# Performance work log

Measured on AMD Instinct MI355X. Metric: run time of the kernel, lower is better.

Reference implementation:

```python
import jax, jax.numpy as jnp
import numpy as np

N = 50000      # number of predictions
E = 1_600_000  # total neighborhood entries (sum of neighborhood sizes)
D = 128        # prediction representation dim
A = 4          # additional per-pair info dim (box offsets / IoU)
H = 128        # block hidden dim


def setup_inputs() -> dict:
    key = jax.random.key(0)
    ks = jax.random.split(key, 16)
    interpolated = jax.random.normal(ks[0], (N, D), dtype=jnp.float32)
    add_info = jax.random.normal(ks[1], (E, A), dtype=jnp.float32)
    neighbor_idx = jax.random.randint(ks[2], (E,), 0, N, dtype=jnp.int32)
    segment_ids = jnp.sort(jax.random.randint(ks[3], (E,), 0, N, dtype=jnp.int32))
    w = lambda k, shape: (jax.random.normal(k, shape, dtype=jnp.float32) * 0.02)
    return {
        "interpolated": interpolated,
        "add_info": add_info,
        "neighbor_idx": neighbor_idx,
        "segment_ids": segment_ids,
        "Wb0": w(ks[4], (D + A, H)), "bb0": jnp.zeros((H,), jnp.float32),
        "Wo0": w(ks[5], (H, D)),     "bo0": jnp.zeros((D,), jnp.float32),
        "Wb1": w(ks[6], (D + A, H)), "bb1": jnp.zeros((H,), jnp.float32),
        "Wo1": w(ks[7], (H, D)),     "bo1": jnp.zeros((D,), jnp.float32),
        "Wf": w(ks[8], (D, 1)),      "bf": jnp.zeros((1,), jnp.float32),
    }


def reference(interpolated, add_info, neighbor_idx, segment_ids,
              Wb0, bb0, Wo0, bo0, Wb1, bb1, Wo1, bo1, Wf, bf):
    def block_step(feats, Wb, bb, Wo, bo):
        # assemble all neighborhoods: gather neighbor reps, concat pair info -> (E, D+A)
        edge_feats = jnp.concatenate([feats[neighbor_idx], add_info], axis=-1)
        # block MLP on neighborhood entries -> (E, H)
        h = jax.nn.relu(edge_feats @ Wb + bb)
        # segment-wise max pool over each prediction's neighborhood -> (N, H)
        pooled = jax.ops.segment_max(h, segment_ids, num_segments=N)
        pooled = jnp.where(jnp.isfinite(pooled), pooled, 0.0)  # empty segments -> 0
        # output projection back to representation space, residual update
        return feats + (pooled @ Wo + bo)

    x = block_step(interpolated, Wb0, bb0, Wo0, bo0)
    x = block_step(x, Wb1, bb1, Wo1, bo1)
    # final layers: compress representation to updated objectness score -> (N, 1)
    return x @ Wf + bf
```

## Files before the change

kernel.cpp:

```cpp
#include <hip/hip_runtime.h>
#include <limits.h>
#include <cstdint>

typedef __bf16 bf16_t;
typedef __attribute__((ext_vector_type(8))) __bf16 bf16x8;
typedef __attribute__((ext_vector_type(4))) float f32x4;
typedef __attribute__((ext_vector_type(2))) float f32x2;

#define CH 64

__device__ __forceinline__ float rlf(float v, int l) {
  return __int_as_float(__builtin_amdgcn_readlane(__float_as_int(v), l));
}

struct PackArgs {
  const float* W[4];
  bf16_t* P[4];
};

__global__ __launch_bounds__(256) void pack4_kernel(PackArgs args) {
  int idx = blockIdx.x * blockDim.x + threadIdx.x;
  int which = idx >> 14;
  int r = idx & 16383;
  int j  = r & 7;
  int L  = (r >> 3) & 63;
  int nt = (r >> 9) & 7;
  int kt = r >> 12;
  int k = kt * 32 + (L >> 4) * 8 + j;
  int n = nt * 16 + (L & 15);
  args.P[which][r] = (bf16_t)args.W[which][(size_t)k * 128 + n];
}

__global__ __launch_bounds__(256, 4) void yproj_f32(
    const float* __restrict__ X, const bf16_t* __restrict__ Wtpk,
    bf16_t* __restrict__ Ybf, float* __restrict__ pooled, int N)
{
  const int tid = threadIdx.x;
  const int base = blockIdx.x * 128;

  float4 z = make_float4(0.f, 0.f, 0.f, 0.f);
  #pragma unroll
  for (int i = 0; i < 16; ++i) {
    int idx = tid + i * 256;
    int row = base + (idx >> 5);
    if (row < N)
      reinterpret_cast<float4*>(pooled)[(size_t)row * 32 + (idx & 31)] = z;
  }

  const int lane = tid & 63;
  const int w    = tid >> 6;
  const int q    = lane >> 4;
  const int ln   = lane & 15;
  const int n0   = base + w * 32;

  int r0 = n0 + ln, r1 = n0 + 16 + ln;
  int r0c = (r0 < N) ? r0 : (N - 1);
  int r1c = (r1 < N) ? r1 : (N - 1);
  const float* x0 = X + (size_t)r0c * 128 + q * 8;
  const float* x1 = X + (size_t)r1c * 128 + q * 8;

  f32x4 acc[2][8];
  #pragma unroll
  for (int mt = 0; mt < 2; ++mt)
    #pragma unroll
    for (int nt = 0; nt < 8; ++nt)
      #pragma unroll
      for (int r = 0; r < 4; ++r) acc[mt][nt][r] = 0.f;

  const bf16x8* Wp = reinterpret_cast<const bf16x8*>(Wtpk);
  #pragma unroll
  for (int kt = 0; kt < 4; ++kt) {
    float4 f0a = *reinterpret_cast<const float4*>(x0 + kt * 32);
    float4 f0b = *reinterpret_cast<const float4*>(x0 + kt * 32 + 4);
    float4 f1a = *reinterpret_cast<const float4*>(x1 + kt * 32);
    float4 f1b = *reinterpret_cast<const float4*>(x1 + kt * 32 + 4);
    bf16x8 a0, a1;
    a0[0] = (bf16_t)f0a.x; a0[1] = (bf16_t)f0a.y; a0[2] = (bf16_t)f0a.z; a0[3] = (bf16_t)f0a.w;
    a0[4] = (bf16_t)f0b.x; a0[5] = (bf16_t)f0b.y; a0[6] = (bf16_t)f0b.z; a0[7] = (bf16_t)f0b.w;
    a1[0] = (bf16_t)f1a.x; a1[1] = (bf16_t)f1a.y; a1[2] = (bf16_t)f1a.z; a1[3] = (bf16_t)f1a.w;
    a1[4] = (bf16_t)f1b.x; a1[5] = (bf16_t)f1b.y; a1[6] = (bf16_t)f1b.z; a1[7] = (bf16_t)f1b.w;
    #pragma unroll
    for (int nt = 0; nt < 8; ++nt) {
      bf16x8 bfrag = Wp[(kt * 8 + nt) * 64 + lane];
      acc[0][nt] = __builtin_amdgcn_mfma_f32_16x16x32_bf16(a0, bfrag, acc[0][nt], 0, 0, 0);
      acc[1][nt] = __builtin_amdgcn_mfma_f32_16x16x32_bf16(a1, bfrag, acc[1][nt], 0, 0, 0);
    }
  }

  #pragma unroll
  for (int mt = 0; mt < 2; ++mt) {
    #pragma unroll
    for (int r = 0; r < 4; ++r) {
      int row = n0 + mt * 16 + q * 4 + r;
      if (row < N) {
        #pragma unroll
        for (int nt = 0; nt < 8; ++nt) {
          int col = nt * 16 + ln;
          Ybf[(size_t)row * 128 + col] = (bf16_t)acc[mt][nt][r];
        }
      }
    }
  }
}

__global__ __launch_bounds__(256, 4) void yproj_bf16(
    const bf16_t* __restrict__ Xbf, const bf16_t* __restrict__ Wtpk,
    bf16_t* __restrict__ Ybf, float* __restrict__ pooled, int N)
{
  const int tid = threadIdx.x;
  const int base = blockIdx.x * 128;

  float4 z = make_float4(0.f, 0.f, 0.f, 0.f);
  #pragma unroll
  for (int i = 0; i < 16; ++i) {
    int idx = tid + i * 256;
    int row = base + (idx >> 5);
    if (row < N)
      reinterpret_cast<float4*>(pooled)[(size_t)row * 32 + (idx & 31)] = z;
  }

  const int lane = tid & 63;
  const int w    = tid >> 6;
  const int q    = lane >> 4;
  const int ln   = lane & 15;
  const int n0   = base + w * 32;

  int r0 = n0 + ln, r1 = n0 + 16 + ln;
  int r0c = (r0 < N) ? r0 : (N - 1);
  int r1c = (r1 < N) ? r1 : (N - 1);
  const bf16_t* x0 = Xbf + (size_t)r0c * 128 + q * 8;
  const bf16_t* x1 = Xbf + (size_t)r1c * 128 + q * 8;

  f32x4 acc[2][8];
  #pragma unroll
  for (int mt = 0; mt < 2; ++mt)
    #pragma unroll
    for (int nt = 0; nt < 8; ++nt)
      #pragma unroll
      for (int r = 0; r < 4; ++r) acc[mt][nt][r] = 0.f;

  const bf16x8* Wp = reinterpret_cast<const bf16x8*>(Wtpk);
  #pragma unroll
  for (int kt = 0; kt < 4; ++kt) {
    bf16x8 a0 = *reinterpret_cast<const bf16x8*>(x0 + kt * 32);
    bf16x8 a1 = *reinterpret_cast<const bf16x8*>(x1 + kt * 32);
    #pragma unroll
    for (int nt = 0; nt < 8; ++nt) {
      bf16x8 bfrag = Wp[(kt * 8 + nt) * 64 + lane];
      acc[0][nt] = __builtin_amdgcn_mfma_f32_16x16x32_bf16(a0, bfrag, acc[0][nt], 0, 0, 0);
      acc[1][nt] = __builtin_amdgcn_mfma_f32_16x16x32_bf16(a1, bfrag, acc[1][nt], 0, 0, 0);
    }
  }

  #pragma unroll
  for (int mt = 0; mt < 2; ++mt) {
    #pragma unroll
    for (int r = 0; r < 4; ++r) {
      int row = n0 + mt * 16 + q * 4 + r;
      if (row < N) {
        #pragma unroll
        for (int nt = 0; nt < 8; ++nt) {
          int col = nt * 16 + ln;
          Ybf[(size_t)row * 128 + col] = (bf16_t)acc[mt][nt][r];
        }
      }
    }
  }
}

__global__ __launch_bounds__(256) void edge_stream(
    const bf16_t* __restrict__ Y,
    const float* __restrict__ Wb,
    const float* __restrict__ bb,
    const float* __restrict__ add_info,
    const int* __restrict__ nbr, const int* __restrict__ segs,
    float* __restrict__ pooled, int E)
{
  const int lane = threadIdx.x & 63;
  const int wv = __builtin_amdgcn_readfirstlane(threadIdx.x >> 6);
  const int e0 = (blockIdx.x * 4 + wv) * CH;
  if (e0 >= E) return;
  const int c0 = lane * 2;

  f32x2 wk[4];
  #pragma unroll
  for (int k = 0; k < 4; ++k) {
    wk[k].x = Wb[(size_t)(128 + k) * 128 + c0];
    wk[k].y = Wb[(size_t)(128 + k) * 128 + c0 + 1];
  }
  f32x2 bbv;
  bbv.x = bb[c0]; bbv.y = bb[c0 + 1];

  unsigned* pooled_u = reinterpret_cast<unsigned*>(pooled);
  f32x2 v; v.x = 0.f; v.y = 0.f;

  if (e0 + CH <= E) {
    int v_nbr = nbr[e0 + lane];
    int v_sg  = segs[e0 + lane];
    float v_ai[4];
    #pragma unroll
    for (int r = 0; r < 4; ++r)
      v_ai[r] = add_info[(size_t)e0 * 4 + r * 64 + lane];

    int cur = __builtin_amdgcn_readlane(v_sg, 0);

    unsigned ybuf[4][8];
    #pragma unroll
    for (int p = 0; p < 3; ++p) {
      #pragma unroll
      for (int j = 0; j < 8; ++j) {
        int rn = __builtin_amdgcn_readlane(v_nbr, p * 8 + j);
        ybuf[p][j] = *((const unsigned*)(Y + (size_t)rn * 128) + lane);
      }
    }

    #pragma unroll
    for (int g = 0; g < CH / 8; ++g) {
      if (g + 3 < CH / 8) {
        #pragma unroll
        for (int j = 0; j < 8; ++j) {
          int rn = __builtin_amdgcn_readlane(v_nbr, (g + 3) * 8 + j);
          ybuf[(g + 3) & 3][j] = *((const unsigned*)(Y + (size_t)rn * 128) + lane);
        }
      }
      #pragma unroll
      for (int j = 0; j < 8; ++j) {
        const int i = g * 8 + j;
        int sg = __builtin_amdgcn_readlane(v_sg, i);
        if (sg != cur) {
          if (v.x > 0.f) atomicMax(&pooled_u[(size_t)cur * 128 + c0], __float_as_uint(v.x));
          if (v.y > 0.f) atomicMax(&pooled_u[(size_t)cur * 128 + c0 + 1], __float_as_uint(v.y));
          v.x = 0.f; v.y = 0.f; cur = sg;
        }
        unsigned yb = ybuf[g & 3][j];
        f32x2 y;
        y.x = __uint_as_float(yb << 16);
        y.y = __uint_as_float(yb & 0xffff0000u);
        float a0 = rlf(v_ai[i >> 4], (i * 4 + 0) & 63);
        float a1 = rlf(v_ai[i >> 4], (i * 4 + 1) & 63);
        float a2 = rlf(v_ai[i >> 4], (i * 4 + 2) & 63);
        float a3 = rlf(v_ai[i >> 4], (i * 4 + 3) & 63);
        f32x2 t = bbv + a0 * wk[0];
        t += a1 * wk[1];
        t += a2 * wk[2];
        t += a3 * wk[3];
        t += y;
        v = __builtin_elementwise_max(v, t);
      }
    }
    if (v.x > 0.f) atomicMax(&pooled_u[(size_t)cur * 128 + c0], __float_as_uint(v.x));
    if (v.y > 0.f) atomicMax(&pooled_u[(size_t)cur * 128 + c0 + 1], __float_as_uint(v.y));
  } else {
    int cur = segs[e0];
    const int rem = E - e0;
    for (int i = 0; i < rem; ++i) {
      const int e = e0 + i;
      int sg = segs[e];
      if (sg != cur) {
        if (v.x > 0.f) atomicMax(&pooled_u[(size_t)cur * 128 + c0], __float_as_uint(v.x));
        if (v.y > 0.f) atomicMax(&pooled_u[(size_t)cur * 128 + c0 + 1], __float_as_uint(v.y));
        v.x = 0.f; v.y = 0.f; cur = sg;
      }
      unsigned yb = *reinterpret_cast<const unsigned*>(Y + (size_t)nbr[e] * 128 + c0);
      float y0 = __uint_as_float(yb << 16);
      float y1 = __uint_as_float(yb & 0xffff0000u);
      const float* ai = add_info + (size_t)e * 4;
      float a0 = ai[0], a1 = ai[1], a2 = ai[2], a3 = ai[3];
      float t0 = y0 + bbv.x + a0 * wk[0].x + a1 * wk[1].x + a2 * wk[2].x + a3 * wk[3].x;
      float t1 = y1 + bbv.y + a0 * wk[0].y + a1 * wk[1].y + a2 * wk[2].y + a3 * wk[3].y;
      v.x = fmaxf(v.x, t0);
      v.y = fmaxf(v.y, t1);
    }
    if (v.x > 0.f) atomicMax(&pooled_u[(size_t)cur * 128 + c0], __float_as_uint(v.x));
    if (v.y > 0.f) atomicMax(&pooled_u[(size_t)cur * 128 + c0 + 1], __float_as_uint(v.y));
  }
}

__global__ __launch_bounds__(256, 4) void update_mfma(
    const float* __restrict__ featsIn, const float* __restrict__ pooled,
    const bf16_t* __restrict__ Wopk, const float* __restrict__ bo,
    float* __restrict__ featsOut, bf16_t* __restrict__ featsOutBf, int N)
{
  const int tid  = threadIdx.x;
  const int lane = tid & 63;
  const int w    = tid >> 6;
  const int q    = lane >> 4;
  const int ln   = lane & 15;
  const int n0   = blockIdx.x * 128 + w * 32;

  int r0 = n0 + ln, r1 = n0 + 16 + ln;
  int r0c = (r0 < N) ? r0 : (N - 1);
  int r1c = (r1 < N) ? r1 : (N - 1);
  const float* p0 = pooled + (size_t)r0c * 128 + q * 8;
  const float* p1 = pooled + (size_t)r1c * 128 + q * 8;

  f32x4 acc[2][8];
  #pragma unroll
  for (int mt = 0; mt < 2; ++mt)
    #pragma unroll
    for (int nt = 0; nt < 8; ++nt)
      #pragma unroll
      for (int r = 0; r < 4; ++r) acc[mt][nt][r] = 0.f;

  const bf16x8* Wp = reinterpret_cast<const bf16x8*>(Wopk);
  #pragma unroll
  for (int kt = 0; kt < 4; ++kt) {
    float4 f0a = *reinterpret_cast<const float4*>(p0 + kt * 32);
    float4 f0b = *reinterpret_cast<const float4*>(p0 + kt * 32 + 4);
    float4 f1a = *reinterpret_cast<const float4*>(p1 + kt * 32);
    float4 f1b = *reinterpret_cast<const float4*>(p1 + kt * 32 + 4);
    bf16x8 a0, a1;
    a0[0] = (bf16_t)f0a.x; a0[1] = (bf16_t)f0a.y; a0[2] = (bf16_t)f0a.z; a0[3] = (bf16_t)f0a.w;
    a0[4] = (bf16_t)f0b.x; a0[5] = (bf16_t)f0b.y; a0[6] = (bf16_t)f0b.z; a0[7] = (bf16_t)f0b.w;
    a1[0] = (bf16_t)f1a.x; a1[1] = (bf16_t)f1a.y; a1[2] = (bf16_t)f1a.z; a1[3] = (bf16_t)f1a.w;
    a1[4] = (bf16_t)f1b.x; a1[5] = (bf16_t)f1b.y; a1[6] = (bf16_t)f1b.z; a1[7] = (bf16_t)f1b.w;
    #pragma unroll
    for (int nt = 0; nt < 8; ++nt) {
      bf16x8 bfrag = Wp[(kt * 8 + nt) * 64 + lane];
      acc[0][nt] = __builtin_amdgcn_mfma_f32_16x16x32_bf16(a0, bfrag, acc[0][nt], 0, 0, 0);
      acc[1][nt] = __builtin_amdgcn_mfma_f32_16x16x32_bf16(a1, bfrag, acc[1][nt], 0, 0, 0);
    }
  }

  float bov[8];
  #pragma unroll
  for (int nt = 0; nt < 8; ++nt) bov[nt] = bo[nt * 16 + ln];

  #pragma unroll
  for (int mt = 0; mt < 2; ++mt) {
    #pragma unroll
    for (int r = 0; r < 4; ++r) {
      int row = n0 + mt * 16 + q * 4 + r;
      if (row < N) {
        #pragma unroll
        for (int nt = 0; nt < 8; ++nt) {
          int col = nt * 16 + ln;
          float o = featsIn[(size_t)row * 128 + col] + acc[mt][nt][r] + bov[nt];
          featsOut[(size_t)row * 128 + col] = o;
          featsOutBf[(size_t)row * 128 + col] = (bf16_t)o;
        }
      }
    }
  }
}

__global__ __launch_bounds__(256, 4) void update_final_mfma(
    const float* __restrict__ featsIn, const float* __restrict__ pooled,
    const bf16_t* __restrict__ Wopk, const float* __restrict__ bo,
    const float* __restrict__ Wf, const float* __restrict__ bf_,
    float* __restrict__ out, int N)
{
  const int tid  = threadIdx.x;
  const int lane = tid & 63;
  const int w    = tid >> 6;
  const int q    = lane >> 4;
  const int ln   = lane & 15;
  const int n0   = blockIdx.x * 128 + w * 32;

  int r0 = n0 + ln, r1 = n0 + 16 + ln;
  int r0c = (r0 < N) ? r0 : (N - 1);
  int r1c = (r1 < N) ? r1 : (N - 1);
  const float* p0 = pooled + (size_t)r0c * 128 + q * 8;
  const float* p1 = pooled + (size_t)r1c * 128 + q * 8;

  f32x4 acc[2][8];
  #pragma unroll
  for (int mt = 0; mt < 2; ++mt)
    #pragma unroll
    for (int nt = 0; nt < 8; ++nt)
      #pragma unroll
      for (int r = 0; r < 4; ++r) acc[mt][nt][r] = 0.f;

  const bf16x8* Wp = reinterpret_cast<const bf16x8*>(Wopk);
  #pragma unroll
  for (int kt = 0; kt < 4; ++kt) {
    float4 f0a = *reinterpret_cast<const float4*>(p0 + kt * 32);
    float4 f0b = *reinterpret_cast<const float4*>(p0 + kt * 32 + 4);
    float4 f1a = *reinterpret_cast<const float4*>(p1 + kt * 32);
    float4 f1b = *reinterpret_cast<const float4*>(p1 + kt * 32 + 4);
    bf16x8 a0, a1;
    a0[0] = (bf16_t)f0a.x; a0[1] = (bf16_t)f0a.y; a0[2] = (bf16_t)f0a.z; a0[3] = (bf16_t)f0a.w;
    a0[4] = (bf16_t)f0b.x; a0[5] = (bf16_t)f0b.y; a0[6] = (bf16_t)f0b.z; a0[7] = (bf16_t)f0b.w;
    a1[0] = (bf16_t)f1a.x; a1[1] = (bf16_t)f1a.y; a1[2] = (bf16_t)f1a.z; a1[3] = (bf16_t)f1a.w;
    a1[4] = (bf16_t)f1b.x; a1[5] = (bf16_t)f1b.y; a1[6] = (bf16_t)f1b.z; a1[7] = (bf16_t)f1b.w;
    #pragma unroll
    for (int nt = 0; nt < 8; ++nt) {
      bf16x8 bfrag = Wp[(kt * 8 + nt) * 64 + lane];
      acc[0][nt] = __builtin_amdgcn_mfma_f32_16x16x32_bf16(a0, bfrag, acc[0][nt], 0, 0, 0);
      acc[1][nt] = __builtin_amdgcn_mfma_f32_16x16x32_bf16(a1, bfrag, acc[1][nt], 0, 0, 0);
    }
  }

  float bov[8], wfv[8];
  #pragma unroll
  for (int nt = 0; nt < 8; ++nt) { bov[nt] = bo[nt * 16 + ln]; wfv[nt] = Wf[nt * 16 + ln]; }
  float bfs = bf_[0];

  #pragma unroll
  for (int mt = 0; mt < 2; ++mt) {
    #pragma unroll
    for (int r = 0; r < 4; ++r) {
      int row = n0 + mt * 16 + q * 4 + r;
      float partial = 0.f;
      if (row < N) {
        #pragma unroll
        for (int nt = 0; nt < 8; ++nt) {
          int col = nt * 16 + ln;
          float o = featsIn[(size_t)row * 128 + col] + acc[mt][nt][r] + bov[nt];
          partial += o * wfv[nt];
        }
      }
      partial += __shfl_xor(partial, 1);
      partial += __shfl_xor(partial, 2);
      partial += __shfl_xor(partial, 4);
      partial += __shfl_xor(partial, 8);
      if (ln == 0 && row < N) out[row] = partial + bfs;
    }
  }
}

extern "C" void kernel_launch(void* const* d_in, const int* in_sizes, int n_in,
                              void* d_out, int out_size, void* d_ws, size_t ws_size,
                              hipStream_t stream)
{
  const float* interpolated = (const float*)d_in[0];
  const float* add_info     = (const float*)d_in[1];
  const int*   nbr          = (const int*)d_in[2];
  const int*   segs         = (const int*)d_in[3];
  const float* Wb0 = (const float*)d_in[4];
  const float* bb0 = (const float*)d_in[5];
  const float* Wo0 = (const float*)d_in[6];
  const float* bo0 = (const float*)d_in[7];
  const float* Wb1 = (const float*)d_in[8];
  const float* bb1 = (const float*)d_in[9];
  const float* Wo1 = (const float*)d_in[10];
  const float* bo1 = (const float*)d_in[11];
  const float* Wf  = (const float*)d_in[12];
  const float* bf_ = (const float*)d_in[13];

  const int N = in_sizes[0] / 128;
  const int E = in_sizes[2];
  float* out = (float*)d_out;

  float* pooled = (float*)d_ws;
  float* featsB = pooled + (size_t)N * 128;
  bf16_t* featsB_bf = (bf16_t*)(featsB + (size_t)N * 128);
  bf16_t* Ybf       = featsB_bf + (size_t)N * 128;
  bf16_t* Wtpk0 = Ybf + (size_t)N * 128;
  bf16_t* Wtpk1 = Wtpk0 + 16384;
  bf16_t* Wopk0 = Wtpk1 + 16384;
  bf16_t* Wopk1 = Wopk0 + 16384;

  const int ugrid = (N + 127) / 128;
  const int egrid = (E + CH * 4 - 1) / (CH * 4);

  PackArgs pa;
  pa.W[0] = Wb0; pa.P[0] = Wtpk0;
  pa.W[1] = Wb1; pa.P[1] = Wtpk1;
  pa.W[2] = Wo0; pa.P[2] = Wopk0;
  pa.W[3] = Wo1; pa.P[3] = Wopk1;
  pack4_kernel<<<256, 256, 0, stream>>>(pa);

  yproj_f32<<<ugrid, 256, 0, stream>>>(interpolated, Wtpk0, Ybf, pooled, N);
  edge_stream<<<egrid, 256, 0, stream>>>(Ybf, Wb0, bb0, add_info, nbr, segs,
                                         pooled, E);
  update_mfma<<<ugrid, 256, 0, stream>>>(interpolated, pooled, Wopk0, bo0,
                                         featsB, featsB_bf, N);

  yproj_bf16<<<ugrid, 256, 0, stream>>>(featsB_bf, Wtpk1, Ybf, pooled, N);
  edge_stream<<<egrid, 256, 0, stream>>>(Ybf, Wb1, bb1, add_info, nbr, segs,
                                         pooled, E);
  update_final_mfma<<<ugrid, 256, 0, stream>>>(featsB, pooled, Wopk1, bo1,
                                               Wf, bf_, out, N);
}
```

Measured before the change: 306.8 us.

## Fold output projections algebraically into next block and final score

Precomputes Wo0·Wb1, a folded bias, and Wo·Wf vectors in a prep kernel. This lets the second block's projection read interpolated and pooled0 directly, and the final score become a dot product over X, pooled0 and pooled1. The change removes both update GEMM kernels and the featsB fp32/bf16 round trip, and replaces them with a fused dual-MFMA projection and a lightweight reduction kernel. In exchange it adds a bf16 rounding of the product weight Wo0·Wb1, which changes numerics slightly, plus a small serial prep GEMM.

```diff
diff --git a/kernel.cpp b/kernel.cpp
--- a/kernel.cpp
+++ b/kernel.cpp
@@ -13,22 +13,66 @@
   return __int_as_float(__builtin_amdgcn_readlane(__float_as_int(v), l));
 }
 
-struct PackArgs {
-  const float* W[4];
-  bf16_t* P[4];
+struct PrepArgs {
+  const float *Wb0, *Wb1, *Wo0, *Wo1, *Wf, *bb1, *bo0, *bo1, *bf;
+  bf16_t *Wt0pk, *Wt1pk, *Wppk;
+  float *bb1p, *wf0p, *wf1p, *cp;
 };
 
-__global__ __launch_bounds__(256) void pack4_kernel(PackArgs args) {
-  int idx = blockIdx.x * blockDim.x + threadIdx.x;
-  int which = idx >> 14;
-  int r = idx & 16383;
-  int j  = r & 7;
-  int L  = (r >> 3) & 63;
-  int nt = (r >> 9) & 7;
-  int kt = r >> 12;
-  int k = kt * 32 + (L >> 4) * 8 + j;
-  int n = nt * 16 + (L & 15);
-  args.P[which][r] = (bf16_t)args.W[which][(size_t)k * 128 + n];
+__global__ __launch_bounds__(256) void prep_kernel(PrepArgs a) {
+  const int blk = blockIdx.x;
+  const int tid = threadIdx.x;
+  if (blk < 128) {
+    int idx = blk * 256 + tid;
+    int which = idx >> 14;
+    int r = idx & 16383;
+    int j  = r & 7;
+    int L  = (r >> 3) & 63;
+    int nt = (r >> 9) & 7;
+    int kt = r >> 12;
+    int k = kt * 32 + (L >> 4) * 8 + j;
+    int n = nt * 16 + (L & 15);
+    const float* W = which ? a.Wb1 : a.Wb0;
+    bf16_t* P = which ? a.Wt1pk : a.Wt0pk;
+    P[r] = (bf16_t)W[(size_t)k * 128 + n];
+  } else if (blk < 136) {
+    int t = (blk - 128) * 256 + tid;
+    int L  = t & 63;
+    int nt = (t >> 6) & 7;
+    int kt = t >> 9;
+    int n = nt * 16 + (L & 15);
+    int kbase = kt * 32 + (L >> 4) * 8;
+    float acc[8];
+    #pragma unroll
+    for (int j = 0; j < 8; ++j) acc[j] = 0.f;
+    for (int m = 0; m < 128; ++m) {
+      float w1 = a.Wb1[(size_t)m * 128 + n];
+      #pragma unroll
+      for (int j = 0; j < 8; ++j)
+        acc[j] += a.Wo0[(size_t)(kbase + j) * 128 + m] * w1;
+    }
+    #pragma unroll
+    for (int j = 0; j < 8; ++j) a.Wppk[(size_t)t * 8 + j] = (bf16_t)acc[j];
+  } else {
+    if (tid < 128) {
+      int n = tid;
+      float s = 0.f;
+      for (int k = 0; k < 128; ++k) s += a.bo0[k] * a.Wb1[(size_t)k * 128 + n];
+      a.bb1p[n] = a.bb1[n] + s;
+      float s0 = 0.f, s1 = 0.f;
+      for (int m = 0; m < 128; ++m) {
+        s0 += a.Wo0[(size_t)n * 128 + m] * a.Wf[m];
+        s1 += a.Wo1[(size_t)n * 128 + m] * a.Wf[m];
+      }
+      a.wf0p[n] = s0;
+      a.wf1p[n] = s1;
+      if (n == 0) {
+        float c = a.bf[0];
+        for (int m = 0; m < 128; ++m) c += (a.bo0[m] + a.bo1[m]) * a.Wf[m];
+        a.cp[0] = c;
+      }
+    }
+  }
 }
 
 __global__ __launch_bounds__(256, 4) void yproj_f32(
@@ -103,9 +147,10 @@
   }
 }
 
-__global__ __launch_bounds__(256, 4) void yproj_bf16(
-    const bf16_t* __restrict__ Xbf, const bf16_t* __restrict__ Wtpk,
-    bf16_t* __restrict__ Ybf, float* __restrict__ pooled, int N)
+__global__ __launch_bounds__(256, 2) void yproj_fused(
+    const float* __restrict__ X, const float* __restrict__ pooled0,
+    const bf16_t* __restrict__ Wtpk, const bf16_t* __restrict__ Wppk,
+    bf16_t* __restrict__ Ybf, float* __restrict__ pooled1, int N)
 {
   const int tid = threadIdx.x;
   const int base = blockIdx.x * 128;
@@ -116,7 +161,7 @@
     int idx = tid + i * 256;
     int row = base + (idx >> 5);
     if (row < N)
-      reinterpret_cast<float4*>(pooled)[(size_t)row * 32 + (idx & 31)] = z;
+      reinterpret_cast<float4*>(pooled1)[(size_t)row * 32 + (idx & 31)] = z;
   }
 
   const int lane = tid & 63;
@@ -128,8 +173,10 @@
   int r0 = n0 + ln, r1 = n0 + 16 + ln;
   int r0c = (r0 < N) ? r0 : (N - 1);
   int r1c = (r1 < N) ? r1 : (N - 1);
-  const bf16_t* x0 = Xbf + (size_t)r0c * 128 + q * 8;
-  const bf16_t* x1 = Xbf + (size_t)r1c * 128 + q * 8;
+  const float* x0 = X + (size_t)r0c * 128 + q * 8;
+  const float* x1 = X + (size_t)r1c * 128 + q * 8;
+  const float* p0 = pooled0 + (size_t)r0c * 128 + q * 8;
+  const float* p1 = pooled0 + (size_t)r1c * 128 + q * 8;
 
   f32x4 acc[2][8];
   #pragma unroll
@@ -139,16 +186,35 @@
       #pragma unroll
       for (int r = 0; r < 4; ++r) acc[mt][nt][r] = 0.f;
 
-  const bf16x8* Wp = reinterpret_cast<const bf16x8*>(Wtpk);
+  const bf16x8* Wt = reinterpret_cast<const bf16x8*>(Wtpk);
+  const bf16x8* Wq = reinterpret_cast<const bf16x8*>(Wppk);
   #pragma unroll
   for (int kt = 0; kt < 4; ++kt) {
-    bf16x8 a0 = *reinterpret_cast<const bf16x8*>(x0 + kt * 32);
-    bf16x8 a1 = *reinterpret_cast<const bf16x8*>(x1 + kt * 32);
+    float4 f0a = *reinterpret_cast<const float4*>(x0 + kt * 32);
+    float4 f0b = *reinterpret_cast<const float4*>(x0 + kt * 32 + 4);
+    float4 f1a = *reinterpret_cast<const float4*>(x1 + kt * 32);
+    float4 f1b = *reinterpret_cast<const float4*>(x1 + kt * 32 + 4);
+    float4 g0a = *reinterpret_cast<const float4*>(p0 + kt * 32);
+    float4 g0b = *reinterpret_cast<const float4*>(p0 + kt * 32 + 4);
+    float4 g1a = *reinterpret_cast<const float4*>(p1 + kt * 32);
+    float4 g1b = *reinterpret_cast<const float4*>(p1 + kt * 32 + 4);
+    bf16x8 a0, a1, b0, b1;
+    a0[0] = (bf16_t)f0a.x; a0[1] = (bf16_t)f0a.y; a0[2] = (bf16_t)f0a.z; a0[3] = (bf16_t)f0a.w;
+    a0[4] = (bf16_t)f0b.x; a0[5] = (bf16_t)f0b.y; a0[6] = (bf16_t)f0b.z; a0[7] = (bf16_t)f0b.w;
+    a1[0] = (bf16_t)f1a.x; a1[1] = (bf16_t)f1a.y; a1[2] = (bf16_t)f1a.z; a1[3] = (bf16_t)f1a.w;
+    a1[4] = (bf16_t)f1b.x; a1[5] = (bf16_t)f1b.y; a1[6] = (bf16_t)f1b.z; a1[7] = (bf16_t)f1b.w;
+    b0[0] = (bf16_t)g0a.x; b0[1] = (bf16_t)g0a.y; b0[2] = (bf16_t)g0a.z; b0[3] = (bf16_t)g0a.w;
+    b0[4] = (bf16_t)g0b.x; b0[5] = (bf16_t)g0b.y; b0[6] = (bf16_t)g0b.z; b0[7] = (bf16_t)g0b.w;
+    b1[0] = (bf16_t)g1a.x; b1[1] = (bf16_t)g1a.y; b1[2] = (bf16_t)g1a.z; b1[3] = (bf16_t)g1a.w;
+    b1[4] = (bf16_t)g1b.x; b1[5] = (bf16_t)g1b.y; b1[6] = (bf16_t)g1b.z; b1[7] = (bf16_t)g1b.w;
     #pragma unroll
     for (int nt = 0; nt < 8; ++nt) {
-      bf16x8 bfrag = Wp[(kt * 8 + nt) * 64 + lane];
-      acc[0][nt] = __builtin_amdgcn_mfma_f32_16x16x32_bf16(a0, bfrag, acc[0][nt], 0, 0, 0);
-      acc[1][nt] = __builtin_amdgcn_mfma_f32_16x16x32_bf16(a1, bfrag, acc[1][nt], 0, 0, 0);
+      bf16x8 wt = Wt[(kt * 8 + nt) * 64 + lane];
+      bf16x8 wq = Wq[(kt * 8 + nt) * 64 + lane];
+      acc[0][nt] = __builtin_amdgcn_mfma_f32_16x16x32_bf16(a0, wt, acc[0][nt], 0, 0, 0);
+      acc[0][nt] = __builtin_amdgcn_mfma_f32_16x16x32_bf16(b0, wq, acc[0][nt], 0, 0, 0);
+      acc[1][nt] = __builtin_amdgcn_mfma_f32_16x16x32_bf16(a1, wt, acc[1][nt], 0, 0, 0);
+      acc[1][nt] = __builtin_amdgcn_mfma_f32_16x16x32_bf16(b1, wq, acc[1][nt], 0, 0, 0);
     }
   }
 
@@ -276,146 +342,30 @@
   }
 }
 
-__global__ __launch_bounds__(256, 4) void update_mfma(
-    const float* __restrict__ featsIn, const float* __restrict__ pooled,
-    const bf16_t* __restrict__ Wopk, const float* __restrict__ bo,
-    float* __restrict__ featsOut, bf16_t* __restrict__ featsOutBf, int N)
+__global__ __launch_bounds__(256) void final3_kernel(
+    const float* __restrict__ X, const float* __restrict__ pooled0,
+    const float* __restrict__ pooled1, const float* __restrict__ Wf,
+    const float* __restrict__ wf0p, const float* __restrict__ wf1p,
+    const float* __restrict__ cp, float* __restrict__ out, int N)
 {
-  const int tid  = threadIdx.x;
-  const int lane = tid & 63;
-  const int w    = tid >> 6;
-  const int q    = lane >> 4;
-  const int ln   = lane & 15;
-  const int n0   = blockIdx.x * 128 + w * 32;
-
-  int r0 = n0 + ln, r1 = n0 + 16 + ln;
-  int r0c = (r0 < N) ? r0 : (N - 1);
-  int r1c = (r1 < N) ? r1 : (N - 1);
-  const float* p0 = pooled + (size_t)r0c * 128 + q * 8;
-  const float* p1 = pooled + (size_t)r1c * 128 + q * 8;
-
-  f32x4 acc[2][8];
-  #pragma unroll
-  for (int mt = 0; mt < 2; ++mt)
-    #pragma unroll
-    for (int nt = 0; nt < 8; ++nt)
-      #pragma unroll
-      for (int r = 0; r < 4; ++r) acc[mt][nt][r] = 0.f;
-
-  const bf16x8* Wp = reinterpret_cast<const bf16x8*>(Wopk);
-  #pragma unroll
-  for (int kt = 0; kt < 4; ++kt) {
-    float4 f0a = *reinterpret_cast<const float4*>(p0 + kt * 32);
-    float4 f0b = *reinterpret_cast<const float4*>(p0 + kt * 32 + 4);
-    float4 f1a = *reinterpret_cast<const float4*>(p1 + kt * 32);
-    float4 f1b = *reinterpret_cast<const float4*>(p1 + kt * 32 + 4);
-    bf16x8 a0, a1;
-    a0[0] = (bf16_t)f0a.x; a0[1] = (bf16_t)f0a.y; a0[2] = (bf16_t)f0a.z; a0[3] = (bf16_t)f0a.w;
-    a0[4] = (bf16_t)f0b.x; a0[5] = (bf16_t)f0b.y; a0[6] = (bf16_t)f0b.z; a0[7] = (bf16_t)f0b.w;
-    a1[0] = (bf16_t)f1a.x; a1[1] = (bf16_t)f1a.y; a1[2] = (bf16_t)f1a.z; a1[3] = (bf16_t)f1a.w;
-    a1[4] = (bf16_t)f1b.x; a1[5] = (bf16_t)f1b.y; a1[6] = (bf16_t)f1b.z; a1[7] = (bf16_t)f1b.w;
-    #pragma unroll
-    for (int nt = 0; nt < 8; ++nt) {
-      bf16x8 bfrag = Wp[(kt * 8 + nt) * 64 + lane];
-      acc[0][nt] = __builtin_amdgcn_mfma_f32_16x16x32_bf16(a0, bfrag, acc[0][nt], 0, 0, 0);
-      acc[1][nt] = __builtin_amdgcn_mfma_f32_16x16x32_bf16(a1, bfrag, acc[1][nt], 0, 0, 0);
-    }
-  }
-
-  float bov[8];
-  #pragma unroll
-  for (int nt = 0; nt < 8; ++nt) bov[nt] = bo[nt * 16 + ln];
-
-  #pragma unroll
-  for (int mt = 0; mt < 2; ++mt) {
-    #pragma unroll
-    for (int r = 0; r < 4; ++r) {
-      int row = n0 + mt * 16 + q * 4 + r;
-      if (row < N) {
-        #pragma unroll
-        for (int nt = 0; nt < 8; ++nt) {
-          int col = nt * 16 + ln;
-          float o = featsIn[(size_t)row * 128 + col] + acc[mt][nt][r] + bov[nt];
-          featsOut[(size_t)row * 128 + col] = o;
-          featsOutBf[(size_t)row * 128 + col] = (bf16_t)o;
-        }
-      }
-    }
-  }
-}
-
-__global__ __launch_bounds__(256, 4) void update_final_mfma(
-    const float* __restrict__ featsIn, const float* __restrict__ pooled,
-    const bf16_t* __restrict__ Wopk, const float* __restrict__ bo,
-    const float* __restrict__ Wf, const float* __restrict__ bf_,
-    float* __restrict__ out, int N)
-{
-  const int tid  = threadIdx.x;
-  const int lane = tid & 63;
-  const int w    = tid >> 6;
-  const int q    = lane >> 4;
-  const int ln   = lane & 15;
-  const int n0   = blockIdx.x * 128 + w * 32;
-
-  int r0 = n0 + ln, r1 = n0 + 16 + ln;
-  int r0c = (r0 < N) ? r0 : (N - 1);
-  int r1c = (r1 < N) ? r1 : (N - 1);
-  const float* p0 = pooled + (size_t)r0c * 128 + q * 8;
-  const float* p1 = pooled + (size_t)r1c * 128 + q * 8;
-
-  f32x4 acc[2][8];
-  #pragma unroll
-  for (int mt = 0; mt < 2; ++mt)
-    #pragma unroll
-    for (int nt = 0; nt < 8; ++nt)
-      #pragma unroll
-      for (int r = 0; r < 4; ++r) acc[mt][nt][r] = 0.f;
-
-  const bf16x8* Wp = reinterpret_cast<const bf16x8*>(Wopk);
-  #pragma unroll
-  for (int kt = 0; kt < 4; ++kt) {
-    float4 f0a = *reinterpret_cast<const float4*>(p0 + kt * 32);
-    float4 f0b = *reinterpret_cast<const float4*>(p0 + kt * 32 + 4);
-    float4 f1a = *reinterpret_cast<const float4*>(p1 + kt * 32);
-    float4 f1b = *reinterpret_cast<const float4*>(p1 + kt * 32 + 4);
-    bf16x8 a0, a1;
-    a0[0] = (bf16_t)f0a.x; a0[1] = (bf16_t)f0a.y; a0[2] = (bf16_t)f0a.z; a0[3] = (bf16_t)f0a.w;
-    a0[4] = (bf16_t)f0b.x; a0[5] = (bf16_t)f0b.y; a0[6] = (bf16_t)f0b.z; a0[7] = (bf16_t)f0b.w;
-    a1[0] = (bf16_t)f1a.x; a1[1] = (bf16_t)f1a.y; a1[2] = (bf16_t)f1a.z; a1[3] = (bf16_t)f1a.w;
-    a1[4] = (bf16_t)f1b.x; a1[5] = (bf16_t)f1b.y; a1[6] = (bf16_t)f1b.z; a1[7] = (bf16_t)f1b.w;
-    #pragma unroll
-    for (int nt = 0; nt < 8; ++nt) {
-      bf16x8 bfrag = Wp[(kt * 8 + nt) * 64 + lane];
-      acc[0][nt] = __builtin_amdgcn_mfma_f32_16x16x32_bf16(a0, bfrag, acc[0][nt], 0, 0, 0);
-      acc[1][nt] = __builtin_amdgcn_mfma_f32_16x16x32_bf16(a1, bfrag, acc[1][nt], 0, 0, 0);
-    }
-  }
-
-  float bov[8], wfv[8];
-  #pragma unroll
-  for (int nt = 0; nt < 8; ++nt) { bov[nt] = bo[nt * 16 + ln]; wfv[nt] = Wf[nt * 16 + ln]; }
-  float bfs = bf_[0];
-
-  #pragma unroll
-  for (int mt = 0; mt < 2; ++mt) {
-    #pragma unroll
-    for (int r = 0; r < 4; ++r) {
-      int row = n0 + mt * 16 + q * 4 + r;
-      float partial = 0.f;
-      if (row < N) {
-        #pragma unroll
-        for (int nt = 0; nt < 8; ++nt) {
-          int col = nt * 16 + ln;
-          float o = featsIn[(size_t)row * 128 + col] + acc[mt][nt][r] + bov[nt];
-          partial += o * wfv[nt];
-        }
-      }
-      partial += __shfl_xor(partial, 1);
-      partial += __shfl_xor(partial, 2);
-      partial += __shfl_xor(partial, 4);
-      partial += __shfl_xor(partial, 8);
-      if (ln == 0 && row < N) out[row] = partial + bfs;
-    }
+  int gtid = blockIdx.x * blockDim.x + threadIdx.x;
+  int wave = gtid >> 6;
+  int lane = threadIdx.x & 63;
+  int nw = (gridDim.x * blockDim.x) >> 6;
+  float w0 = Wf[lane],   w1 = Wf[64 + lane];
+  float u0 = wf0p[lane], u1 = wf0p[64 + lane];
+  float t0 = wf1p[lane], t1 = wf1p[64 + lane];
+  float c = cp[0];
+  for (int n = wave; n < N; n += nw) {
+    const float* xr = X + (size_t)n * 128;
+    const float* p0 = pooled0 + (size_t)n * 128;
+    const float* p1 = pooled1 + (size_t)n * 128;
+    float v = xr[lane] * w0 + xr[64 + lane] * w1
+            + p0[lane] * u0 + p0[64 + lane] * u1
+            + p1[lane] * t0 + p1[64 + lane] * t1;
+    #pragma unroll
+    for (int off = 32; off > 0; off >>= 1) v += __shfl_down(v, off);
+    if (lane == 0) out[n] = v + c;
   }
 }
 
@@ -442,34 +392,36 @@
   const int E = in_sizes[2];
   float* out = (float*)d_out;
 
-  float* pooled = (float*)d_ws;
-  float* featsB = pooled + (size_t)N * 128;
-  bf16_t* featsB_bf = (bf16_t*)(featsB + (size_t)N * 128);
-  bf16_t* Ybf       = featsB_bf + (size_t)N * 128;
-  bf16_t* Wtpk0 = Ybf + (size_t)N * 128;
-  bf16_t* Wtpk1 = Wtpk0 + 16384;
-  bf16_t* Wopk0 = Wtpk1 + 16384;
-  bf16_t* Wopk1 = Wopk0 + 16384;
+  float* pooled0 = (float*)d_ws;
+  float* pooled1 = pooled0 + (size_t)N * 128;
+  bf16_t* Ybf    = (bf16_t*)(pooled1 + (size_t)N * 128);
+  bf16_t* Wt0pk  = Ybf + (size_t)N * 128;
+  bf16_t* Wt1pk  = Wt0pk + 16384;
+  bf16_t* Wppk   = Wt1pk + 16384;
+  float* bb1p    = (float*)(Wppk + 16384);
+  float* wf0p    = bb1p + 128;
+  float* wf1p    = wf0p + 128;
+  float* cp      = wf1p + 128;
 
   const int ugrid = (N + 127) / 128;
   const int egrid = (E + CH * 4 - 1) / (CH * 4);
 
-  PackArgs pa;
-  pa.W[0] = Wb0; pa.P[0] = Wtpk0;
-  pa.W[1] = Wb1; pa.P[1] = Wtpk1;
-  pa.W[2] = Wo0; pa.P[2] = Wopk0;
-  pa.W[3] = Wo1; pa.P[3] = Wopk1;
-  pack4_kernel<<<256, 256, 0, stream>>>(pa);
-
-  yproj_f32<<<ugrid, 256, 0, stream>>>(interpolated, Wtpk0, Ybf, pooled, N);
+  PrepArgs pa;
+  pa.Wb0 = Wb0; pa.Wb1 = Wb1; pa.Wo0 = Wo0; pa.Wo1 = Wo1; pa.Wf = Wf;
+  pa.bb1 = bb1; pa.bo0 = bo0; pa.bo1 = bo1; pa.bf = bf_;
+  pa.Wt0pk = Wt0pk; pa.Wt1pk = Wt1pk; pa.Wppk = Wppk;
+  pa.bb1p = bb1p; pa.wf0p = wf0p; pa.wf1p = wf1p; pa.cp = cp;
+  prep_kernel<<<137, 256, 0, stream>>>(pa);
+
+  yproj_f32<<<ugrid, 256, 0, stream>>>(interpolated, Wt0pk, Ybf, pooled0, N);
   edge_stream<<<egrid, 256, 0, stream>>>(Ybf, Wb0, bb0, add_info, nbr, segs,
-                                         pooled, E);
-  update_mfma<<<ugrid, 256, 0, stream>>>(interpolated, pooled, Wopk0, bo0,
-                                         featsB, featsB_bf, N);
-
-  yproj_bf16<<<ugrid, 256, 0, stream>>>(featsB_bf, Wtpk1, Ybf, pooled, N);
-  edge_stream<<<egrid, 256, 0, stream>>>(Ybf, Wb1, bb1, add_info, nbr, segs,
-                                         pooled, E);
-  update_final_mfma<<<ugrid, 256, 0, stream>>>(featsB, pooled, Wopk1, bo1,
-                                               Wf, bf_, out, N);
-}
+                                         pooled0, E);
+
+  yproj_fused<<<ugrid, 256, 0, stream>>>(interpolated, pooled0, Wt1pk, Wppk,
+                                         Ybf, pooled1, N);
+  edge_stream<<<egrid, 256, 0, stream>>>(Ybf, Wb1, bb1p, add_info, nbr, segs,
+                                         pooled1, E);
+
+  final3_kernel<<<512, 256, 0, stream>>>(interpolated, pooled0, pooled1,
+                                         Wf, wf0p, wf1p, cp, out, N);
+}
```

New measurement: 307.6 us. No clear change (+0.2%).
